# Kernel tuning notes

Measured on AMD Instinct MI355X. Metric: run time of the kernel, lower is better.

## Reference

```python
import jax, jax.numpy as jnp
import numpy as np

B, D, L = 16, 256, 200
T = 1000   # max_frame_length
K = 3      # kernel_size
DW, DC = 4, 2


def setup_inputs() -> dict:
    key = jax.random.key(0)
    ks = jax.random.split(key, 16)
    plen = jax.random.randint(ks[0], (B,), 150, L + 1)
    pm = jnp.arange(L)[None, :] < plen[:, None]              # (B,L) True=valid
    phoneme_mask = pm[:, None, :]                            # (B,1,L)
    durations = jax.random.uniform(ks[1], (B, L), minval=1.0, maxval=8.0) * pm
    phoneme = jax.random.normal(ks[2], (B, D, L), dtype=jnp.float32)
    s = 0.05
    params = {
        'Wpw': jax.random.normal(ks[3], (D, D)) * s, 'bpw': jnp.zeros((D,)),
        'Cw': jax.random.normal(ks[4], (8, D, K)) * s, 'cbw': jnp.zeros((8,)),
        'Mw': jax.random.normal(ks[5], (10, DW)) * s, 'mbw': jnp.zeros((DW,)),
        'Lw': jax.random.normal(ks[6], (DW * D, D)) * s, 'lbw': jnp.zeros((D,)),
        'Wpc': jax.random.normal(ks[7], (D, D)) * s, 'bpc': jnp.zeros((D,)),
        'Cc': jax.random.normal(ks[8], (8, D, K)) * s, 'cbc': jnp.zeros((8,)),
        'Mc': jax.random.normal(ks[9], (10, DC)) * s, 'mbc': jnp.zeros((DC,)),
        'Lc': jax.random.normal(ks[10], (DW * DC, D)) * s, 'lbc': jnp.zeros((D,)),
        'Wo': jax.random.normal(ks[11], (D, 2 * D)) * s, 'bo': jnp.zeros((2 * D,)),
    }
    return {'durations': durations, 'phoneme': phoneme, 'phoneme_mask': phoneme_mask, **params}


def _conv_swish(x, W1, b1, Ck, cb, pm):
    # 1x1 conv (proj) then kernel-K 'same' conv then SiLU; mask padded phones
    h = jnp.einsum('od,bdl->bol', W1, x) + b1[None, :, None]
    h = jax.lax.conv_general_dilated(h, Ck, (1,), 'SAME',
                                     dimension_numbers=('NCH', 'OIH', 'NCH')) + cb[None, :, None]
    h = jax.nn.silu(h)
    h = jnp.where(pm[:, None, :], h, 0.0)
    return h.transpose(0, 2, 1)  # (B, L, 8)


def _mlp(S, E, h, M, mb):
    # concat start/end boundary scalars with per-phone conv features -> (B,T,L,10)
    feat = jnp.concatenate([S[..., None], E[..., None],
                            jnp.broadcast_to(h[:, None], (B, T, L, 8))], axis=-1)
    return jax.nn.silu(feat @ M + mb)


def _forward(durations, phoneme, phoneme_mask, Wpw, bpw, Cw, cbw, Mw, mbw, Lw, lbw,
             Wpc, bpc, Cc, cbc, Mc, mbc, Lc, lbc, Wo, bo):
    pm = phoneme_mask[:, 0, :]                                          # (B,L)
    frame_lengths = jnp.clip(jnp.round(durations.sum(-1)).astype(jnp.int32), 0, T)
    frame_mask = jnp.arange(T)[None, :] < frame_lengths[:, None]        # (B,T)
    attn_mask = frame_mask[:, :, None] & pm[:, None, :]                 # (B,T,L)
    sd = jnp.cumsum(durations, axis=-1)                                 # (B,L)
    sk = sd - durations
    t = jnp.arange(1, T + 1, dtype=durations.dtype)
    S = jnp.where(attn_mask, t[None, :, None] - sk[:, None, :], 0.0)    # (B,T,L)
    E = jnp.where(attn_mask, (sd - sk)[:, None, :], 0.0)                # (B,T,L)

    h_w = _conv_swish(phoneme, Wpw, bpw, Cw, cbw, pm)
    w = _mlp(S, E, h_w, Mw, mbw)                                        # (B,T,L,DW)
    w = jnp.where(pm[:, None, :, None], w, -jnp.inf)
    w = jax.nn.softmax(w, axis=2)                                       # softmax over phones
    w = jnp.where(frame_mask[:, :, None, None], w, 0.0)

    h_c = _conv_swish(phoneme, Wpc, bpc, Cc, cbc, pm)
    c = _mlp(S, E, h_c, Mc, mbc)                                        # (B,T,L,DC)

    wh = jnp.einsum('btlq,bdl->btqd', w, phoneme).reshape(B, T, DW * D) @ Lw + lbw
    wc = jnp.einsum('btlq,btlp->btqp', w, c).reshape(B, T, DW * DC) @ Lc + lbc
    whc = jnp.where(frame_mask[..., None], wh + wc, 0.0)                # (B,T,D)
    out = (whc @ Wo + bo).transpose(0, 2, 1)                            # (B,2D,T)
    return out, frame_mask, frame_lengths, w.transpose(0, 3, 1, 2)


def reference(durations, phoneme, phoneme_mask, Wpw, bpw, Cw, cbw, Mw, mbw, Lw, lbw,
              Wpc, bpc, Cc, cbc, Mc, mbc, Lc, lbc, Wo, bo):
    out, frame_mask, frame_lengths, w = _forward(
        durations, phoneme, phoneme_mask, Wpw, bpw, Cw, cbw, Mw, mbw, Lw, lbw,
        Wpc, bpc, Cc, cbc, Mc, mbc, Lc, lbc, Wo, bo)
    mean, log_std = jnp.split(out, 2, axis=1)                           # (B,D,T) each
    return (mean, log_std, frame_mask, frame_lengths, w)
```

## Files before the change

kernel.cpp:

```cpp
#include <hip/hip_runtime.h>
#include <hip/hip_bf16.h>
#include <math.h>

#define NB 16
#define ND 256
#define NL 200
#define NT 1000

typedef unsigned short ushort_t;
typedef __bf16 bf16x8 __attribute__((ext_vector_type(8)));
typedef float f32x4 __attribute__((ext_vector_type(4)));

#define OFF_FL    4981936u
#define OFF_GT    11535552u
#define OFF_WOT   15221952u
#define OFF_BASE  15287488u

__device__ __forceinline__ float silu_f(float x){ return x / (1.f + __expf(-x)); }
__device__ __forceinline__ ushort_t f2bf(float x){
  __hip_bfloat16 h = __float2bfloat16(x);
  return *(ushort_t*)&h;
}

__global__ __launch_bounds__(256, 2) void k_A(
    const float* __restrict__ dur, const float* __restrict__ ph,
    const float* __restrict__ Wp_w, const float* __restrict__ C_w, const float* __restrict__ bp_w,
    const float* __restrict__ Wp_c, const float* __restrict__ C_c, const float* __restrict__ bp_c,
    const float* __restrict__ Wo, const float* __restrict__ Lw,
    const float* __restrict__ cbw, const float* __restrict__ cbc,
    const float* __restrict__ Mw, const float* __restrict__ mbw,
    const float* __restrict__ Mc, const float* __restrict__ mbc,
    int* __restrict__ fl_ws, float* __restrict__ o_fm, float* __restrict__ o_fl,
    ushort_t* __restrict__ WoT, float4* __restrict__ base,
    ushort_t* __restrict__ Gt)
{
  __shared__ __align__(16) unsigned char smem[69632];
  int bid = blockIdx.x, tid = threadIdx.x;

  if (bid < 256){
    int r = bid;
    int b = r >> 4, x = r & 15;
    if (x >= 13){
      int l0 = 208 + (x - 13)*16;
      if (tid < 32)
        base[((size_t)(b*256 + l0 + (tid >> 1)))*2 + (tid & 1)] = make_float4(0,0,0,0);
      return;
    }
    float* sdur = (float*)smem;
    float* ssk  = sdur + 256;
    float (*phs)[256] = (float (*)[256])(ssk + 256);
    float (*Uw)[20] = (float (*)[20])((float*)phs + 18*256);
    float (*Uc)[20] = Uw + 256;
    float (*sh)[17] = (float (*)[17])(Uc + 256*1);
    sh = (float (*)[17])((float*)Uc + 256*20);
    int l0 = x*16;

    if (tid < NL) sdur[tid] = dur[b*NL + tid];
    __syncthreads();
    if (tid == 0){
      float run = 0.f;
      for (int l = 0; l < NL; ++l){ ssk[l] = run; run += sdur[l]; }
    }
    {
      int d = tid;
      const float* pr = ph + ((size_t)b*ND + d)*NL;
      #pragma unroll
      for (int j = 0; j < 18; ++j){
        int l = l0 - 1 + j;
        phs[j][d] = (l >= 0 && l < NL) ? pr[l] : 0.f;
      }
    }
    __syncthreads();
    {
      int i = tid;
      float uw[18], uc[18];
      float bw = bp_w[i], bc = bp_c[i];
      #pragma unroll
      for (int j = 0; j < 18; ++j){ uw[j] = bw; uc[j] = bc; }
      const float4* wr = (const float4*)(Wp_w + (size_t)i*ND);
      const float4* cr = (const float4*)(Wp_c + (size_t)i*ND);
      for (int d4 = 0; d4 < 64; ++d4){
        float4 a = wr[d4], c = cr[d4];
        #pragma unroll
        for (int j = 0; j < 18; ++j){
          float4 p = *(const float4*)&phs[j][d4*4];
          uw[j] += a.x*p.x + a.y*p.y + a.z*p.z + a.w*p.w;
          uc[j] += c.x*p.x + c.y*p.y + c.z*p.z + c.w*p.w;
        }
      }
      #pragma unroll
      for (int j = 0; j < 18; ++j){
        int l = l0 - 1 + j;
        bool pad = (l < 0 || l >= NL);
        Uw[i][j] = pad ? 0.f : uw[j];
        Uc[i][j] = pad ? 0.f : uc[j];
      }
    }
    __syncthreads();
    {
      int lu = tid >> 4, u = tid & 15;
      int l = l0 + lu;
      float h = 0.f;
      if (l < NL){
        int branch = u >> 3, oc = u & 7;
        float (*U)[20] = branch ? Uc : Uw;
        const float* C = branch ? C_c : C_w;
        float val = (branch ? cbc : cbw)[oc];
        #pragma unroll 4
        for (int i = 0; i < ND; ++i){
          const float* cc = C + ((size_t)oc*ND + i)*3;
          val += cc[0]*U[i][lu] + cc[1]*U[i][lu + 1] + cc[2]*U[i][lu + 2];
        }
        float pm = (sdur[l] > 0.5f) ? 1.f : 0.f;
        h = silu_f(val) * pm;
      }
      sh[lu][u] = h;
    }
    __syncthreads();
    if (tid < 16){
      int ll = x*16 + tid;
      float4 o0 = make_float4(0,0,0,0);
      float4 o1 = make_float4(0,0,0,0);
      if (ll < NL){
        float dl  = sdur[ll];
        float pm  = (dl > 0.5f) ? 1.f : 0.f;
        float skl = ssk[ll];
        float c1[4], c2[2];
        #pragma unroll
        for (int q = 0; q < 4; ++q) c1[q] = mbw[q] + dl*Mw[4 + q] - skl*Mw[q];
        #pragma unroll
        for (int p = 0; p < 2; ++p) c2[p] = mbc[p] + dl*Mc[2 + p] - skl*Mc[p];
        #pragma unroll
        for (int j = 0; j < 8; ++j){
          float hwv = sh[tid][j], hcv = sh[tid][8 + j];
          #pragma unroll
          for (int q = 0; q < 4; ++q) c1[q] += hwv*Mw[(2 + j)*4 + q];
          #pragma unroll
          for (int p = 0; p < 2; ++p) c2[p] += hcv*Mc[(2 + j)*2 + p];
        }
        o0 = make_float4(c1[0], c1[1], c1[2], c1[3]);
        o1 = make_float4(c2[0], c2[1], pm, 0.f);
      }
      base[((size_t)(b*256 + ll))*2 + 0] = o0;
      base[((size_t)(b*256 + ll))*2 + 1] = o1;
    }
  } else if (bid < 512){
    int r = bid - 256;
    int xb = r & 1, yb = (r >> 1) & 1, bq = r >> 2;
    int b = bq >> 2, q = bq & 3;
    int m0 = yb * 128;
    int n0 = xb * 128;
    int lane = tid & 63, wave = tid >> 6;
    int wm = wave >> 1, wn = wave & 1;
    int col = lane & 15, kg4 = lane >> 4;
    ushort_t (*Asub)[136] = (ushort_t (*)[136])smem;
    ushort_t (*Bsub)[136] = (ushort_t (*)[136])(smem + 34816);

    f32x4 acc[4][4] = {};
    for (int kh = 0; kh < 2; ++kh){
      int d0 = kh*128;
      if (tid < 128){
        int n = m0 + tid;
        const float* src = Lw + ((size_t)(q*256 + d0))*ND + n;
        #pragma unroll
        for (int dc = 0; dc < 16; ++dc){
          ushort_t tmp[8];
          #pragma unroll
          for (int j = 0; j < 8; ++j)
            tmp[j] = f2bf(src[(size_t)(dc*8 + j)*ND]);
          *(uint4*)&Asub[tid][dc*8] = *(const uint4*)tmp;
        }
      } else {
        int t2 = tid - 128;
        int l = n0 + t2;
        if (l < NL){
          const float* src = ph + ((size_t)b*ND + d0)*NL + l;
          #pragma unroll
          for (int dc = 0; dc < 16; ++dc){
            ushort_t tmp[8];
            #pragma unroll
            for (int j = 0; j < 8; ++j)
              tmp[j] = f2bf(src[(size_t)(dc*8 + j)*NL]);
            *(uint4*)&Bsub[t2][dc*8] = *(const uint4*)tmp;
          }
        } else {
          uint4 z; z.x = z.y = z.z = z.w = 0u;
          #pragma unroll
          for (int dc = 0; dc < 16; ++dc) *(uint4*)&Bsub[t2][dc*8] = z;
        }
      }
      __syncthreads();
      for (int kt = 0; kt < 4; ++kt){
        int k0 = kt*32;
        bf16x8 afr[4], bfr[4];
        #pragma unroll
        for (int i = 0; i < 4; ++i)
          afr[i] = *(const bf16x8*)&Asub[wm*64 + i*16 + col][k0 + kg4*8];
        #pragma unroll
        for (int j = 0; j < 4; ++j)
          bfr[j] = *(const bf16x8*)&Bsub[wn*64 + j*16 + col][k0 + kg4*8];
        #pragma unroll
        for (int i = 0; i < 4; ++i)
          #pragma unroll
          for (int j = 0; j < 4; ++j)
            acc[i][j] = __builtin_amdgcn_mfma_f32_16x16x32_bf16(afr[i], bfr[j], acc[i][j], 0, 0, 0);
      }
      __syncthreads();
    }
    ushort_t (*st2)[136] = Asub;
    int rq = lane >> 4;
    #pragma unroll
    for (int i = 0; i < 4; ++i){
      #pragma unroll
      for (int rr = 0; rr < 4; ++rr){
        int rl = wm*64 + i*16 + rq*4 + rr;
        #pragma unroll
        for (int j = 0; j < 4; ++j){
          int cl = wn*64 + j*16 + col;
          st2[rl][cl] = f2bf(acc[i][j][rr]);
        }
      }
    }
    __syncthreads();
    #pragma unroll
    for (int rep = 0; rep < 8; ++rep){
      int row = rep*16 + (tid >> 4);
      int ch  = tid & 15;
      int l   = n0 + ch*8;
      if (l < NL){
        int n = m0 + row;
        *(uint4*)(Gt + ((size_t)(b*ND + n))*800 + q*NL + l) = *(const uint4*)&st2[row][ch*8];
      }
    }
  } else if (bid < 528){
    int b = bid - 512;
    float* sdur = (float*)smem;
    int* sfl = (int*)(sdur + 256);
    if (tid < NL) sdur[tid] = dur[b*NL + tid];
    __syncthreads();
    if (tid == 0){
      float run = 0.f;
      for (int l = 0; l < NL; ++l) run += sdur[l];
      int fl = (int)rintf(run);
      fl = fl < 0 ? 0 : (fl > NT ? NT : fl);
      sfl[0] = fl; fl_ws[b] = fl; o_fl[b] = (float)fl;
    }
    __syncthreads();
    int flv = sfl[0];
    for (int t = tid; t < NT; t += 256) o_fm[b*NT + t] = (t < flv) ? 1.f : 0.f;
  } else {
    int base_id = (bid - 528)*256 + tid;
    #pragma unroll
    for (int rep = 0; rep < 4; ++rep){
      int gid = rep*32768 + base_id;
      int n = gid >> 8, k = gid & 255;
      WoT[gid] = f2bf(Wo[(size_t)k*512 + n]);
    }
  }
}

#define AP 808
#define TT 64
__global__ __launch_bounds__(1024, 4) void k_wv_fused(
    const float4* __restrict__ base,
    const int* __restrict__ fl_ws,
    const float* __restrict__ Mw, const float* __restrict__ Mc,
    const ushort_t* __restrict__ Gt,
    const float* __restrict__ Lc,
    const float* __restrict__ lbc,
    const float* __restrict__ lbw,
    const ushort_t* __restrict__ WoT,
    const float* __restrict__ bo,
    float* __restrict__ wout,
    float* __restrict__ o_mean, float* __restrict__ o_lstd)
{
  __shared__ ushort_t As[TT*AP];
  __shared__ float    wcs[TT][8];
  int b = blockIdx.x;
  int m0 = blockIdx.y * TT;
  int tid = threadIdx.x, lane = tid & 63, wave = tid >> 6;
  int col = lane & 15, kg4 = lane >> 4;
  int fl = fl_ws[b];

  if (fl <= m0){
    for (int idx = tid; idx < TT*4*50; idx += 1024){
      int tl = idx / 200;
      int rqs = idx - tl*200;
      int q = rqs / 50, seg = rqs - q*50;
      int t = m0 + tl;
      if (t < NT)
        *(float4*)&wout[(((size_t)(b*4 + q))*NT + t)*NL + seg*4] = make_float4(0,0,0,0);
    }
    for (int idx = tid; idx < 512*16; idx += 1024){
      int s = idx >> 4, j = idx & 15;
      int t0 = m0 + j*4;
      if (t0 + 3 < NT){
        float v = bo[s];
        float4 v4 = make_float4(v, v, v, v);
        if (s < ND) *(float4*)&o_mean[((size_t)b*ND + s)*NT + t0] = v4;
        else        *(float4*)&o_lstd[((size_t)b*ND + (s - ND))*NT + t0] = v4;
      }
    }
    return;
  }

  int l0 = lane*4;
  bool lv = (l0 < NL);

  #pragma unroll
  for (int s = 0; s < 4; ++s){
    int tl = wave*4 + s, t = m0 + tl;
    if (t < fl) continue;
    for (int k = l0; k < 800; k += 256){
      uint2 zz2; zz2.x = 0u; zz2.y = 0u;
      *(uint2*)&As[tl*AP + k] = zz2;
    }
    if (lane < 8) wcs[tl][lane] = 0.f;
    if (t < NT && lv){
      float4 z4 = make_float4(0,0,0,0);
      #pragma unroll
      for (int q = 0; q < 4; ++q)
        *(float4*)&wout[(((size_t)(b*4 + q))*NT + t)*NL + l0] = z4;
    }
  }

  float b0a[4][4], b1x[4], b1y[4], pmv[4];
  #pragma unroll
  for (int e = 0; e < 4; ++e){
    float4 v0 = make_float4(0,0,0,0), v1 = make_float4(0,0,0,0);
    if (lv){
      v0 = base[((size_t)(b*256 + l0 + e))*2 + 0];
      v1 = base[((size_t)(b*256 + l0 + e))*2 + 1];
    }
    b0a[e][0] = v0.x; b0a[e][1] = v0.y; b0a[e][2] = v0.z; b0a[e][3] = v0.w;
    b1x[e] = v1.x; b1y[e] = v1.y; pmv[e] = v1.z;
  }
  float mwq[4] = {Mw[0], Mw[1], Mw[2], Mw[3]};
  float mcp[2] = {Mc[0], Mc[1]};

  for (int sp = 0; sp < 2; ++sp){
    int tl0 = wave*4 + sp*2;
    int t0 = m0 + tl0;
    if (t0 >= fl) break;
    bool a1 = (t0 + 1 < fl);
    float tf[2] = {(float)(t0 + 1), (float)(t0 + 2)};

    float z[2][4][4], mx[2][4];
    #pragma unroll
    for (int u = 0; u < 2; ++u)
      #pragma unroll
      for (int q = 0; q < 4; ++q) mx[u][q] = -INFINITY;
    #pragma unroll
    for (int e = 0; e < 4; ++e){
      #pragma unroll
      for (int u = 0; u < 2; ++u){
        #pragma unroll
        for (int q = 0; q < 4; ++q){
          float sv = silu_f(b0a[e][q] + tf[u]*mwq[q]);
          float zv = (pmv[e] > 0.f) ? sv : -INFINITY;
          z[u][e][q] = zv;
          mx[u][q] = fmaxf(mx[u][q], zv);
        }
      }
    }
    #pragma unroll
    for (int u = 0; u < 2; ++u)
      #pragma unroll
      for (int q = 0; q < 4; ++q){
        float v = mx[u][q];
        #pragma unroll
        for (int off = 32; off; off >>= 1) v = fmaxf(v, __shfl_xor(v, off));
        mx[u][q] = v;
      }
    float is4[2][4] = {{0,0,0,0},{0,0,0,0}};
    #pragma unroll
    for (int e = 0; e < 4; ++e){
      #pragma unroll
      for (int u = 0; u < 2; ++u){
        #pragma unroll
        for (int q = 0; q < 4; ++q){
          float ev = (pmv[e] > 0.f) ? __expf(z[u][e][q] - mx[u][q]) : 0.f;
          z[u][e][q] = ev;
          is4[u][q] += ev;
        }
      }
    }
    #pragma unroll
    for (int u = 0; u < 2; ++u)
      #pragma unroll
      for (int q = 0; q < 4; ++q){
        float v = is4[u][q];
        #pragma unroll
        for (int off = 32; off; off >>= 1) v += __shfl_xor(v, off);
        is4[u][q] = 1.f / v;
      }
    float cv[2][4][2];
    #pragma unroll
    for (int e = 0; e < 4; ++e)
      #pragma unroll
      for (int u = 0; u < 2; ++u){
        cv[u][e][0] = silu_f(b1x[e] + tf[u]*mcp[0]);
        cv[u][e][1] = silu_f(b1y[e] + tf[u]*mcp[1]);
      }
    float wc[2][8];
    #pragma unroll
    for (int u = 0; u < 2; ++u)
      #pragma unroll
      for (int x = 0; x < 8; ++x) wc[u][x] = 0.f;
    #pragma unroll
    for (int u = 0; u < 2; ++u){
      bool act = (u == 0) || a1;
      int t = t0 + u, tl = tl0 + u;
      #pragma unroll
      for (int q = 0; q < 4; ++q){
        float w0 = z[u][0][q]*is4[u][q];
        float w1 = z[u][1][q]*is4[u][q];
        float w2 = z[u][2][q]*is4[u][q];
        float w3 = z[u][3][q]*is4[u][q];
        if (act && lv){
          *(float4*)&wout[(((size_t)(b*4 + q))*NT + t)*NL + l0] =
              make_float4(w0, w1, w2, w3);
          uint2 pk;
          pk.x = (unsigned)f2bf(w0) | ((unsigned)f2bf(w1) << 16);
          pk.y = (unsigned)f2bf(w2) | ((unsigned)f2bf(w3) << 16);
          *(uint2*)&As[tl*AP + q*NL + l0] = pk;
        }
        wc[u][q*2 + 0] += w0*cv[u][0][0] + w1*cv[u][1][0] + w2*cv[u][2][0] + w3*cv[u][3][0];
        wc[u][q*2 + 1] += w0*cv[u][0][1] + w1*cv[u][1][1] + w2*cv[u][2][1] + w3*cv[u][3][1];
      }
    }
    #pragma unroll
    for (int u = 0; u < 2; ++u){
      if (u == 1 && !a1) break;
      #pragma unroll
      for (int x = 0; x < 8; ++x){
        float v = wc[u][x];
        #pragma unroll
        for (int off = 32; off; off >>= 1) v += __shfl_xor(v, off);
        wc[u][x] = v;
      }
      if (lane == 0){
        #pragma unroll
        for (int x = 0; x < 8; ++x) wcs[tl0 + u][x] = wc[u][x];
      }
    }
  }
  __syncthreads();

  f32x4 acc[4] = {};
  const ushort_t* Gb = Gt + (size_t)b*ND*800;
  for (int kt = 0; kt < 25; ++kt){
    int k0 = kt*32;
    bf16x8 afr[4], bfr;
    #pragma unroll
    for (int i = 0; i < 4; ++i)
      afr[i] = *(const bf16x8*)(&As[(i*16 + col)*AP + k0 + kg4*8]);
    bfr = *(const bf16x8*)(Gb + ((size_t)(wave*16 + col))*800 + k0 + kg4*8);
    #pragma unroll
    for (int i = 0; i < 4; ++i)
      acc[i] = __builtin_amdgcn_mfma_f32_16x16x32_bf16(afr[i], bfr, acc[i], 0, 0, 0);
  }
  __syncthreads();

  ushort_t (*stc)[264] = (ushort_t (*)[264])As;
  {
    int rq = lane >> 4;
    int n = wave*16 + col;
    float lbn = lbc[n], lbwn = lbw[n];
    float lcn[8];
    #pragma unroll
    for (int u = 0; u < 8; ++u) lcn[u] = Lc[u*ND + n];
    #pragma unroll
    for (int i = 0; i < 4; ++i){
      #pragma unroll
      for (int r = 0; r < 4; ++r){
        int tl = i*16 + rq*4 + r;
        int t = m0 + tl;
        if (t < NT){
          float f = (t < fl) ? 1.f : 0.f;
          float vcv = lbn
            + wcs[tl][0]*lcn[0] + wcs[tl][1]*lcn[1]
            + wcs[tl][2]*lcn[2] + wcs[tl][3]*lcn[3]
            + wcs[tl][4]*lcn[4] + wcs[tl][5]*lcn[5]
            + wcs[tl][6]*lcn[6] + wcs[tl][7]*lcn[7];
          stc[tl][n] = f2bf(f * (acc[i][r] + lbwn + vcv));
        }
      }
    }
  }
  __syncthreads();

  {
    f32x4 acc2[2][4] = {};
    for (int kt = 0; kt < 8; ++kt){
      int k0 = kt*32;
      bf16x8 afr[2], bfr[4];
      #pragma unroll
      for (int j = 0; j < 4; ++j)
        bfr[j] = *(const bf16x8*)(&stc[j*16 + col][k0 + kg4*8]);
      #pragma unroll
      for (int i = 0; i < 2; ++i)
        afr[i] = *(const bf16x8*)(WoT + ((size_t)(wave*32 + i*16 + col))*ND + k0 + kg4*8);
      #pragma unroll
      for (int i = 0; i < 2; ++i)
        #pragma unroll
        for (int j = 0; j < 4; ++j)
          acc2[i][j] = __builtin_amdgcn_mfma_f32_16x16x32_bf16(afr[i], bfr[j], acc2[i][j], 0, 0, 0);
    }
    int rq = lane >> 4;
    #pragma unroll
    for (int i = 0; i < 2; ++i){
      #pragma unroll
      for (int r = 0; r < 4; ++r){
        int s = wave*32 + i*16 + rq*4 + r;
        float bov = bo[s];
        #pragma unroll
        for (int j = 0; j < 4; ++j){
          int t = m0 + j*16 + col;
          if (t < NT){
            float v = acc2[i][j][r] + bov;
            if (s < ND) o_mean[((size_t)b*ND + s)*NT + t] = v;
            else        o_lstd[((size_t)b*ND + (s - ND))*NT + t] = v;
          }
        }
      }
    }
  }
}

extern "C" void kernel_launch(void* const* d_in, const int* in_sizes, int n_in,
                              void* d_out, int out_size, void* d_ws, size_t ws_size,
                              hipStream_t stream)
{
  const float* dur = (const float*)d_in[0];
  const float* ph  = (const float*)d_in[1];
  const float* Wpw = (const float*)d_in[3];
  const float* bpw = (const float*)d_in[4];
  const float* Cw  = (const float*)d_in[5];
  const float* cbw = (const float*)d_in[6];
  const float* Mw  = (const float*)d_in[7];
  const float* mbw = (const float*)d_in[8];
  const float* Lw  = (const float*)d_in[9];
  const float* lbw = (const float*)d_in[10];
  const float* Wpc = (const float*)d_in[11];
  const float* bpc = (const float*)d_in[12];
  const float* Cc  = (const float*)d_in[13];
  const float* cbc = (const float*)d_in[14];
  const float* Mc  = (const float*)d_in[15];
  const float* mbc = (const float*)d_in[16];
  const float* Lc  = (const float*)d_in[17];
  const float* lbc = (const float*)d_in[18];
  const float* Wo  = (const float*)d_in[19];
  const float* bo  = (const float*)d_in[20];

  float* out    = (float*)d_out;
  float* o_mean = out;
  float* o_lstd = out + (size_t)NB*ND*NT;
  float* o_fm   = o_lstd + (size_t)NB*ND*NT;
  float* o_fl   = o_fm + NB*NT;
  float* o_w    = o_fl + NB;

  float* ws   = (float*)d_ws;
  int*   fl   = (int*)(ws + OFF_FL);
  ushort_t* Gt   = (ushort_t*)(ws + OFF_GT);
  ushort_t* WoT  = (ushort_t*)(ws + OFF_WOT);
  float4*   base = (float4*)(ws + OFF_BASE);

  k_A<<<656, 256, 0, stream>>>(dur, ph, Wpw, Cw, bpw, Wpc, Cc, bpc, Wo, Lw,
                               cbw, cbc, Mw, mbw, Mc, mbc,
                               fl, o_fm, o_fl, WoT, base, Gt);
  {
    dim3 g(NB, 16);
    k_wv_fused<<<g, 1024, 0, stream>>>(base, fl, Mw, Mc, Gt, Lc, lbc, lbw,
                                       WoT, bo, o_w, o_mean, o_lstd);
  }
}
```

Before: 237.9 us.

## Replace static grid with atomic work queue per XCD in fused kernel

The fused attention/projection kernel moves from a fixed (batch, tile) grid to 256 persistent blocks. Each block pulls (batch, time-tile) work items from one of eight atomic counters, chosen by blockIdx&7 so each queue is likely served by a single XCD. The aim is to balance load across blocks, since tiles past the frame length are cheap, and to keep each batch's Gt data in one XCD's L2. In exchange it adds a memset launch, an atomic plus two barriers per work item, and a dependence on how blocks are mapped to XCDs.

```diff
diff --git a/kernel.cpp b/kernel.cpp
--- a/kernel.cpp
+++ b/kernel.cpp
@@ -12,6 +12,7 @@
 typedef float f32x4 __attribute__((ext_vector_type(4)));
 
 #define OFF_FL    4981936u
+#define OFF_QC    4982000u
 #define OFF_GT    11535552u
 #define OFF_WOT   15221952u
 #define OFF_BASE  15287488u
@@ -51,8 +52,7 @@
     float (*phs)[256] = (float (*)[256])(ssk + 256);
     float (*Uw)[20] = (float (*)[20])((float*)phs + 18*256);
     float (*Uc)[20] = Uw + 256;
-    float (*sh)[17] = (float (*)[17])(Uc + 256*1);
-    sh = (float (*)[17])((float*)Uc + 256*20);
+    float (*sh)[17] = (float (*)[17])((float*)Uc + 256*20);
     int l0 = x*16;
 
     if (tid < NL) sdur[tid] = dur[b*NL + tid];
@@ -271,256 +271,267 @@
     const float* __restrict__ lbw,
     const ushort_t* __restrict__ WoT,
     const float* __restrict__ bo,
+    unsigned* __restrict__ qctr,
     float* __restrict__ wout,
     float* __restrict__ o_mean, float* __restrict__ o_lstd)
 {
   __shared__ ushort_t As[TT*AP];
   __shared__ float    wcs[TT][8];
-  int b = blockIdx.x;
-  int m0 = blockIdx.y * TT;
+  __shared__ int      s_idx;
   int tid = threadIdx.x, lane = tid & 63, wave = tid >> 6;
   int col = lane & 15, kg4 = lane >> 4;
-  int fl = fl_ws[b];
-
-  if (fl <= m0){
-    for (int idx = tid; idx < TT*4*50; idx += 1024){
-      int tl = idx / 200;
-      int rqs = idx - tl*200;
-      int q = rqs / 50, seg = rqs - q*50;
-      int t = m0 + tl;
-      if (t < NT)
-        *(float4*)&wout[(((size_t)(b*4 + q))*NT + t)*NL + seg*4] = make_float4(0,0,0,0);
-    }
-    for (int idx = tid; idx < 512*16; idx += 1024){
-      int s = idx >> 4, j = idx & 15;
-      int t0 = m0 + j*4;
-      if (t0 + 3 < NT){
-        float v = bo[s];
-        float4 v4 = make_float4(v, v, v, v);
-        if (s < ND) *(float4*)&o_mean[((size_t)b*ND + s)*NT + t0] = v4;
-        else        *(float4*)&o_lstd[((size_t)b*ND + (s - ND))*NT + t0] = v4;
-      }
-    }
-    return;
-  }
-
-  int l0 = lane*4;
-  bool lv = (l0 < NL);
-
-  #pragma unroll
-  for (int s = 0; s < 4; ++s){
-    int tl = wave*4 + s, t = m0 + tl;
-    if (t < fl) continue;
-    for (int k = l0; k < 800; k += 256){
-      uint2 zz2; zz2.x = 0u; zz2.y = 0u;
-      *(uint2*)&As[tl*AP + k] = zz2;
-    }
-    if (lane < 8) wcs[tl][lane] = 0.f;
-    if (t < NT && lv){
-      float4 z4 = make_float4(0,0,0,0);
-      #pragma unroll
-      for (int q = 0; q < 4; ++q)
-        *(float4*)&wout[(((size_t)(b*4 + q))*NT + t)*NL + l0] = z4;
-    }
-  }
-
-  float b0a[4][4], b1x[4], b1y[4], pmv[4];
-  #pragma unroll
-  for (int e = 0; e < 4; ++e){
-    float4 v0 = make_float4(0,0,0,0), v1 = make_float4(0,0,0,0);
-    if (lv){
-      v0 = base[((size_t)(b*256 + l0 + e))*2 + 0];
-      v1 = base[((size_t)(b*256 + l0 + e))*2 + 1];
-    }
-    b0a[e][0] = v0.x; b0a[e][1] = v0.y; b0a[e][2] = v0.z; b0a[e][3] = v0.w;
-    b1x[e] = v1.x; b1y[e] = v1.y; pmv[e] = v1.z;
-  }
-  float mwq[4] = {Mw[0], Mw[1], Mw[2], Mw[3]};
-  float mcp[2] = {Mc[0], Mc[1]};
-
-  for (int sp = 0; sp < 2; ++sp){
-    int tl0 = wave*4 + sp*2;
-    int t0 = m0 + tl0;
-    if (t0 >= fl) break;
-    bool a1 = (t0 + 1 < fl);
-    float tf[2] = {(float)(t0 + 1), (float)(t0 + 2)};
-
-    float z[2][4][4], mx[2][4];
+  int xq = blockIdx.x & 7;
+
+  for (;;){
+    __syncthreads();
+    if (tid == 0) s_idx = (int)atomicAdd(&qctr[xq], 1u);
+    __syncthreads();
+    int idx = s_idx;
+    if (idx >= 32) break;
+    int b  = xq + ((idx >> 4) << 3);
+    int m0 = (idx & 15) * TT;
+    int fl = fl_ws[b];
+
+    if (fl <= m0){
+      for (int i2 = tid; i2 < TT*4*50; i2 += 1024){
+        int tl = i2 / 200;
+        int rqs = i2 - tl*200;
+        int q = rqs / 50, seg = rqs - q*50;
+        int t = m0 + tl;
+        if (t < NT)
+          *(float4*)&wout[(((size_t)(b*4 + q))*NT + t)*NL + seg*4] = make_float4(0,0,0,0);
+      }
+      for (int i2 = tid; i2 < 512*16; i2 += 1024){
+        int s = i2 >> 4, j = i2 & 15;
+        int t0 = m0 + j*4;
+        if (t0 + 3 < NT){
+          float v = bo[s];
+          float4 v4 = make_float4(v, v, v, v);
+          if (s < ND) *(float4*)&o_mean[((size_t)b*ND + s)*NT + t0] = v4;
+          else        *(float4*)&o_lstd[((size_t)b*ND + (s - ND))*NT + t0] = v4;
+        }
+      }
+      continue;
+    }
+
+    int l0 = lane*4;
+    bool lv = (l0 < NL);
+
     #pragma unroll
-    for (int u = 0; u < 2; ++u)
-      #pragma unroll
-      for (int q = 0; q < 4; ++q) mx[u][q] = -INFINITY;
+    for (int s = 0; s < 4; ++s){
+      int tl = wave*4 + s, t = m0 + tl;
+      if (t < fl) continue;
+      for (int k = l0; k < 800; k += 256){
+        uint2 zz2; zz2.x = 0u; zz2.y = 0u;
+        *(uint2*)&As[tl*AP + k] = zz2;
+      }
+      if (lane < 8) wcs[tl][lane] = 0.f;
+      if (t < NT && lv){
+        float4 z4 = make_float4(0,0,0,0);
+        #pragma unroll
+        for (int q = 0; q < 4; ++q)
+          *(float4*)&wout[(((size_t)(b*4 + q))*NT + t)*NL + l0] = z4;
+      }
+    }
+
+    float b0a[4][4], b1x[4], b1y[4], pmv[4];
     #pragma unroll
     for (int e = 0; e < 4; ++e){
+      float4 v0 = make_float4(0,0,0,0), v1 = make_float4(0,0,0,0);
+      if (lv){
+        v0 = base[((size_t)(b*256 + l0 + e))*2 + 0];
+        v1 = base[((size_t)(b*256 + l0 + e))*2 + 1];
+      }
+      b0a[e][0] = v0.x; b0a[e][1] = v0.y; b0a[e][2] = v0.z; b0a[e][3] = v0.w;
+      b1x[e] = v1.x; b1y[e] = v1.y; pmv[e] = v1.z;
+    }
+    float mwq[4] = {Mw[0], Mw[1], Mw[2], Mw[3]};
+    float mcp[2] = {Mc[0], Mc[1]};
+
+    for (int sp = 0; sp < 2; ++sp){
+      int tl0 = wave*4 + sp*2;
+      int t0 = m0 + tl0;
+      if (t0 >= fl) break;
+      bool a1 = (t0 + 1 < fl);
+      float tf[2] = {(float)(t0 + 1), (float)(t0 + 2)};
+
+      float z[2][4][4], mx[2][4];
+      #pragma unroll
+      for (int u = 0; u < 2; ++u)
+        #pragma unroll
+        for (int q = 0; q < 4; ++q) mx[u][q] = -INFINITY;
+      #pragma unroll
+      for (int e = 0; e < 4; ++e){
+        #pragma unroll
+        for (int u = 0; u < 2; ++u){
+          #pragma unroll
+          for (int q = 0; q < 4; ++q){
+            float sv = silu_f(b0a[e][q] + tf[u]*mwq[q]);
+            float zv = (pmv[e] > 0.f) ? sv : -INFINITY;
+            z[u][e][q] = zv;
+            mx[u][q] = fmaxf(mx[u][q], zv);
+          }
+        }
+      }
+      #pragma unroll
+      for (int u = 0; u < 2; ++u)
+        #pragma unroll
+        for (int q = 0; q < 4; ++q){
+          float v = mx[u][q];
+          #pragma unroll
+          for (int off = 32; off; off >>= 1) v = fmaxf(v, __shfl_xor(v, off));
+          mx[u][q] = v;
+        }
+      float is4[2][4] = {{0,0,0,0},{0,0,0,0}};
+      #pragma unroll
+      for (int e = 0; e < 4; ++e){
+        #pragma unroll
+        for (int u = 0; u < 2; ++u){
+          #pragma unroll
+          for (int q = 0; q < 4; ++q){
+            float ev = (pmv[e] > 0.f) ? __expf(z[u][e][q] - mx[u][q]) : 0.f;
+            z[u][e][q] = ev;
+            is4[u][q] += ev;
+          }
+        }
+      }
+      #pragma unroll
+      for (int u = 0; u < 2; ++u)
+        #pragma unroll
+        for (int q = 0; q < 4; ++q){
+          float v = is4[u][q];
+          #pragma unroll
+          for (int off = 32; off; off >>= 1) v += __shfl_xor(v, off);
+          is4[u][q] = 1.f / v;
+        }
+      float cv[2][4][2];
+      #pragma unroll
+      for (int e = 0; e < 4; ++e)
+        #pragma unroll
+        for (int u = 0; u < 2; ++u){
+          cv[u][e][0] = silu_f(b1x[e] + tf[u]*mcp[0]);
+          cv[u][e][1] = silu_f(b1y[e] + tf[u]*mcp[1]);
+        }
+      float wc[2][8];
+      #pragma unroll
+      for (int u = 0; u < 2; ++u)
+        #pragma unroll
+        for (int x = 0; x < 8; ++x) wc[u][x] = 0.f;
       #pragma unroll
       for (int u = 0; u < 2; ++u){
+        bool act = (u == 0) || a1;
+        int t = t0 + u, tl = tl0 + u;
         #pragma unroll
         for (int q = 0; q < 4; ++q){
-          float sv = silu_f(b0a[e][q] + tf[u]*mwq[q]);
-          float zv = (pmv[e] > 0.f) ? sv : -INFINITY;
-          z[u][e][q] = zv;
-          mx[u][q] = fmaxf(mx[u][q], zv);
-        }
-      }
-    }
-    #pragma unroll
-    for (int u = 0; u < 2; ++u)
-      #pragma unroll
-      for (int q = 0; q < 4; ++q){
-        float v = mx[u][q];
-        #pragma unroll
-        for (int off = 32; off; off >>= 1) v = fmaxf(v, __shfl_xor(v, off));
-        mx[u][q] = v;
-      }
-    float is4[2][4] = {{0,0,0,0},{0,0,0,0}};
-    #pragma unroll
-    for (int e = 0; e < 4; ++e){
+          float w0 = z[u][0][q]*is4[u][q];
+          float w1 = z[u][1][q]*is4[u][q];
+          float w2 = z[u][2][q]*is4[u][q];
+          float w3 = z[u][3][q]*is4[u][q];
+          if (act && lv){
+            *(float4*)&wout[(((size_t)(b*4 + q))*NT + t)*NL + l0] =
+                make_float4(w0, w1, w2, w3);
+            uint2 pk;
+            pk.x = (unsigned)f2bf(w0) | ((unsigned)f2bf(w1) << 16);
+            pk.y = (unsigned)f2bf(w2) | ((unsigned)f2bf(w3) << 16);
+            *(uint2*)&As[tl*AP + q*NL + l0] = pk;
+          }
+          wc[u][q*2 + 0] += w0*cv[u][0][0] + w1*cv[u][1][0] + w2*cv[u][2][0] + w3*cv[u][3][0];
+          wc[u][q*2 + 1] += w0*cv[u][0][1] + w1*cv[u][1][1] + w2*cv[u][2][1] + w3*cv[u][3][1];
+        }
+      }
       #pragma unroll
       for (int u = 0; u < 2; ++u){
-        #pragma unroll
-        for (int q = 0; q < 4; ++q){
-          float ev = (pmv[e] > 0.f) ? __expf(z[u][e][q] - mx[u][q]) : 0.f;
-          z[u][e][q] = ev;
-          is4[u][q] += ev;
-        }
-      }
-    }
-    #pragma unroll
-    for (int u = 0; u < 2; ++u)
-      #pragma unroll
-      for (int q = 0; q < 4; ++q){
-        float v = is4[u][q];
-        #pragma unroll
-        for (int off = 32; off; off >>= 1) v += __shfl_xor(v, off);
-        is4[u][q] = 1.f / v;
-      }
-    float cv[2][4][2];
-    #pragma unroll
-    for (int e = 0; e < 4; ++e)
-      #pragma unroll
-      for (int u = 0; u < 2; ++u){
-        cv[u][e][0] = silu_f(b1x[e] + tf[u]*mcp[0]);
-        cv[u][e][1] = silu_f(b1y[e] + tf[u]*mcp[1]);
-      }
-    float wc[2][8];
-    #pragma unroll
-    for (int u = 0; u < 2; ++u)
-      #pragma unroll
-      for (int x = 0; x < 8; ++x) wc[u][x] = 0.f;
-    #pragma unroll
-    for (int u = 0; u < 2; ++u){
-      bool act = (u == 0) || a1;
-      int t = t0 + u, tl = tl0 + u;
-      #pragma unroll
-      for (int q = 0; q < 4; ++q){
-        float w0 = z[u][0][q]*is4[u][q];
-        float w1 = z[u][1][q]*is4[u][q];
-        float w2 = z[u][2][q]*is4[u][q];
-        float w3 = z[u][3][q]*is4[u][q];
-        if (act && lv){
-          *(float4*)&wout[(((size_t)(b*4 + q))*NT + t)*NL + l0] =
-              make_float4(w0, w1, w2, w3);
-          uint2 pk;
-          pk.x = (unsigned)f2bf(w0) | ((unsigned)f2bf(w1) << 16);
-          pk.y = (unsigned)f2bf(w2) | ((unsigned)f2bf(w3) << 16);
-          *(uint2*)&As[tl*AP + q*NL + l0] = pk;
-        }
-        wc[u][q*2 + 0] += w0*cv[u][0][0] + w1*cv[u][1][0] + w2*cv[u][2][0] + w3*cv[u][3][0];
-        wc[u][q*2 + 1] += w0*cv[u][0][1] + w1*cv[u][1][1] + w2*cv[u][2][1] + w3*cv[u][3][1];
-      }
-    }
-    #pragma unroll
-    for (int u = 0; u < 2; ++u){
-      if (u == 1 && !a1) break;
-      #pragma unroll
-      for (int x = 0; x < 8; ++x){
-        float v = wc[u][x];
-        #pragma unroll
-        for (int off = 32; off; off >>= 1) v += __shfl_xor(v, off);
-        wc[u][x] = v;
-      }
-      if (lane == 0){
-        #pragma unroll
-        for (int x = 0; x < 8; ++x) wcs[tl0 + u][x] = wc[u][x];
-      }
-    }
-  }
-  __syncthreads();
-
-  f32x4 acc[4] = {};
-  const ushort_t* Gb = Gt + (size_t)b*ND*800;
-  for (int kt = 0; kt < 25; ++kt){
-    int k0 = kt*32;
-    bf16x8 afr[4], bfr;
-    #pragma unroll
-    for (int i = 0; i < 4; ++i)
-      afr[i] = *(const bf16x8*)(&As[(i*16 + col)*AP + k0 + kg4*8]);
-    bfr = *(const bf16x8*)(Gb + ((size_t)(wave*16 + col))*800 + k0 + kg4*8);
-    #pragma unroll
-    for (int i = 0; i < 4; ++i)
-      acc[i] = __builtin_amdgcn_mfma_f32_16x16x32_bf16(afr[i], bfr, acc[i], 0, 0, 0);
-  }
-  __syncthreads();
-
-  ushort_t (*stc)[264] = (ushort_t (*)[264])As;
-  {
-    int rq = lane >> 4;
-    int n = wave*16 + col;
-    float lbn = lbc[n], lbwn = lbw[n];
-    float lcn[8];
-    #pragma unroll
-    for (int u = 0; u < 8; ++u) lcn[u] = Lc[u*ND + n];
-    #pragma unroll
-    for (int i = 0; i < 4; ++i){
-      #pragma unroll
-      for (int r = 0; r < 4; ++r){
-        int tl = i*16 + rq*4 + r;
-        int t = m0 + tl;
-        if (t < NT){
-          float f = (t < fl) ? 1.f : 0.f;
-          float vcv = lbn
-            + wcs[tl][0]*lcn[0] + wcs[tl][1]*lcn[1]
-            + wcs[tl][2]*lcn[2] + wcs[tl][3]*lcn[3]
-            + wcs[tl][4]*lcn[4] + wcs[tl][5]*lcn[5]
-            + wcs[tl][6]*lcn[6] + wcs[tl][7]*lcn[7];
-          stc[tl][n] = f2bf(f * (acc[i][r] + lbwn + vcv));
-        }
-      }
-    }
-  }
-  __syncthreads();
-
-  {
-    f32x4 acc2[2][4] = {};
-    for (int kt = 0; kt < 8; ++kt){
+        if (u == 1 && !a1) break;
+        #pragma unroll
+        for (int x = 0; x < 8; ++x){
+          float v = wc[u][x];
+          #pragma unroll
+          for (int off = 32; off; off >>= 1) v += __shfl_xor(v, off);
+          wc[u][x] = v;
+        }
+        if (lane == 0){
+          #pragma unroll
+          for (int x = 0; x < 8; ++x) wcs[tl0 + u][x] = wc[u][x];
+        }
+      }
+    }
+    __syncthreads();
+
+    f32x4 acc[4] = {};
+    const ushort_t* Gb = Gt + (size_t)b*ND*800;
+    for (int kt = 0; kt < 25; ++kt){
       int k0 = kt*32;
-      bf16x8 afr[2], bfr[4];
-      #pragma unroll
-      for (int j = 0; j < 4; ++j)
-        bfr[j] = *(const bf16x8*)(&stc[j*16 + col][k0 + kg4*8]);
-      #pragma unroll
-      for (int i = 0; i < 2; ++i)
-        afr[i] = *(const bf16x8*)(WoT + ((size_t)(wave*32 + i*16 + col))*ND + k0 + kg4*8);
-      #pragma unroll
-      for (int i = 0; i < 2; ++i)
+      bf16x8 afr[4], bfr;
+      #pragma unroll
+      for (int i = 0; i < 4; ++i)
+        afr[i] = *(const bf16x8*)(&As[(i*16 + col)*AP + k0 + kg4*8]);
+      bfr = *(const bf16x8*)(Gb + ((size_t)(wave*16 + col))*800 + k0 + kg4*8);
+      #pragma unroll
+      for (int i = 0; i < 4; ++i)
+        acc[i] = __builtin_amdgcn_mfma_f32_16x16x32_bf16(afr[i], bfr, acc[i], 0, 0, 0);
+    }
+    __syncthreads();
+
+    ushort_t (*stc)[264] = (ushort_t (*)[264])As;
+    {
+      int rq = lane >> 4;
+      int n = wave*16 + col;
+      float lbn = lbc[n], lbwn = lbw[n];
+      float lcn[8];
+      #pragma unroll
+      for (int u = 0; u < 8; ++u) lcn[u] = Lc[u*ND + n];
+      #pragma unroll
+      for (int i = 0; i < 4; ++i){
+        #pragma unroll
+        for (int r = 0; r < 4; ++r){
+          int tl = i*16 + rq*4 + r;
+          int t = m0 + tl;
+          if (t < NT){
+            float f = (t < fl) ? 1.f : 0.f;
+            float vcv = lbn
+              + wcs[tl][0]*lcn[0] + wcs[tl][1]*lcn[1]
+              + wcs[tl][2]*lcn[2] + wcs[tl][3]*lcn[3]
+              + wcs[tl][4]*lcn[4] + wcs[tl][5]*lcn[5]
+              + wcs[tl][6]*lcn[6] + wcs[tl][7]*lcn[7];
+            stc[tl][n] = f2bf(f * (acc[i][r] + lbwn + vcv));
+          }
+        }
+      }
+    }
+    __syncthreads();
+
+    {
+      f32x4 acc2[2][4] = {};
+      for (int kt = 0; kt < 8; ++kt){
+        int k0 = kt*32;
+        bf16x8 afr[2], bfr[4];
         #pragma unroll
         for (int j = 0; j < 4; ++j)
-          acc2[i][j] = __builtin_amdgcn_mfma_f32_16x16x32_bf16(afr[i], bfr[j], acc2[i][j], 0, 0, 0);
-    }
-    int rq = lane >> 4;
-    #pragma unroll
-    for (int i = 0; i < 2; ++i){
-      #pragma unroll
-      for (int r = 0; r < 4; ++r){
-        int s = wave*32 + i*16 + rq*4 + r;
-        float bov = bo[s];
-        #pragma unroll
-        for (int j = 0; j < 4; ++j){
-          int t = m0 + j*16 + col;
-          if (t < NT){
-            float v = acc2[i][j][r] + bov;
-            if (s < ND) o_mean[((size_t)b*ND + s)*NT + t] = v;
-            else        o_lstd[((size_t)b*ND + (s - ND))*NT + t] = v;
+          bfr[j] = *(const bf16x8*)(&stc[j*16 + col][k0 + kg4*8]);
+        #pragma unroll
+        for (int i = 0; i < 2; ++i)
+          afr[i] = *(const bf16x8*)(WoT + ((size_t)(wave*32 + i*16 + col))*ND + k0 + kg4*8);
+        #pragma unroll
+        for (int i = 0; i < 2; ++i)
+          #pragma unroll
+          for (int j = 0; j < 4; ++j)
+            acc2[i][j] = __builtin_amdgcn_mfma_f32_16x16x32_bf16(afr[i], bfr[j], acc2[i][j], 0, 0, 0);
+      }
+      int rq = lane >> 4;
+      #pragma unroll
+      for (int i = 0; i < 2; ++i){
+        #pragma unroll
+        for (int r = 0; r < 4; ++r){
+          int s = wave*32 + i*16 + rq*4 + r;
+          float bov = bo[s];
+          #pragma unroll
+          for (int j = 0; j < 4; ++j){
+            int t = m0 + j*16 + col;
+            if (t < NT){
+              float v = acc2[i][j][r] + bov;
+              if (s < ND) o_mean[((size_t)b*ND + s)*NT + t] = v;
+              else        o_lstd[((size_t)b*ND + (s - ND))*NT + t] = v;
+            }
           }
         }
       }
@@ -562,16 +573,16 @@
 
   float* ws   = (float*)d_ws;
   int*   fl   = (int*)(ws + OFF_FL);
+  unsigned* qctr = (unsigned*)(ws + OFF_QC);
   ushort_t* Gt   = (ushort_t*)(ws + OFF_GT);
   ushort_t* WoT  = (ushort_t*)(ws + OFF_WOT);
   float4*   base = (float4*)(ws + OFF_BASE);
 
+  hipMemsetAsync(qctr, 0, 8*sizeof(unsigned), stream);
+
   k_A<<<656, 256, 0, stream>>>(dur, ph, Wpw, Cw, bpw, Wpc, Cc, bpc, Wo, Lw,
                                cbw, cbc, Mw, mbw, Mc, mbc,
                                fl, o_fm, o_fl, WoT, base, Gt);
-  {
-    dim3 g(NB, 16);
-    k_wv_fused<<<g, 1024, 0, stream>>>(base, fl, Mw, Mc, Gt, Lc, lbc, lbw,
-                                       WoT, bo, o_w, o_mean, o_lstd);
-  }
+  k_wv_fused<<<256, 1024, 0, stream>>>(base, fl, Mw, Mc, Gt, Lc, lbc, lbw,
+                                       WoT, bo, qctr, o_w, o_mean, o_lstd);
 }
```

New measurement: 255.8 us. 1.08x slower.
